# Kernel tuning notes

Hardware: AMD Instinct MI355X
Metric: run time of the kernel (lower is better)

## Reference

```python
import jax, jax.numpy as jnp
import numpy as np

B, T, C = 8, 2048, 512   # batch, seq_len, channels (= output_size for residual)
H, K, D = 4, 128, 128    # heads, key_size, per-head value size
KS, DIL = 4, 4           # conv kernel size, dilation = kernal_size**block_id
BAND = 3                 # matrix_band_part num_lower = num_upper = 3
NEG = -10000000.0


def setup_inputs() -> dict:
    key = jax.random.key(0)
    ks = jax.random.split(key, 12)
    s = 0.02
    f32 = jnp.float32
    x = jax.random.normal(ks[0], (B, T, C), f32)
    # per-head q/k/v dense params (stacked over head axis)
    Wq = jax.random.normal(ks[1], (H, C, K), f32) * s
    bq = jnp.zeros((H, K), f32)
    Wk = jax.random.normal(ks[2], (H, C, K), f32) * s
    bk = jnp.zeros((H, K), f32)
    Wv = jax.random.normal(ks[3], (H, C, D), f32) * s
    bv = jnp.zeros((H, D), f32)
    # output combiner Dense(output_size)
    Wo = jax.random.normal(ks[4], (H * D, C), f32) * s
    bo = jnp.zeros((C,), f32)
    # causal dilated Conv1D: kernel layout WIO = (kernel, in, out)
    Wc = jax.random.normal(ks[5], (KS, C, C), f32) * s
    bc = jnp.zeros((C,), f32)
    return {"x": x, "Wq": Wq, "bq": bq, "Wk": Wk, "bk": bk,
            "Wv": Wv, "bv": bv, "Wo": Wo, "bo": bo, "Wc": Wc, "bc": bc}


def reference(x, Wq, bq, Wk, bk, Wv, bv, Wo, bo, Wc, bc):
    # per-head projections: [B,H,T,K/D]
    q = jnp.einsum('btc,hck->bhtk', x, Wq) + bq[None, :, None, :]
    k = jnp.einsum('btc,hck->bhtk', x, Wk) + bk[None, :, None, :]
    v = jnp.einsum('btc,hcd->bhtd', x, Wv) + bv[None, :, None, :]
    # dense scores then band mask (faithful to matrix_band_part + abs>0 mask)
    sim = jnp.einsum('bhtk,bhsk->bhts', q, k) / jnp.sqrt(jnp.float32(K))
    idx = jnp.arange(T)
    band = (jnp.abs(idx[:, None] - idx[None, :]) <= BAND).astype(sim.dtype)
    simb = sim * band
    mask = jnp.where(jnp.abs(simb) > 0.0, 0.0, 1.0).astype(sim.dtype)
    att = jax.nn.softmax(simb + NEG * mask, axis=-1)
    heads = jnp.einsum('bhts,bhsd->bhtd', att, v)          # [B,H,T,D]
    cat = heads.transpose(0, 2, 1, 3).reshape(B, T, H * D)  # concat heads
    out = cat @ Wo + bo                                     # Dense(512)
    # causal dilated conv + relu
    pad = (KS - 1) * DIL
    conv = jax.lax.conv_general_dilated(
        out, Wc, window_strides=(1,), padding=[(pad, 0)],
        rhs_dilation=(DIL,), dimension_numbers=('NWC', 'WIO', 'NWC'))
    conv = jax.nn.relu(conv + bc)
    res = conv + x
    return jnp.where(res >= 0, res, 0.2 * res)  # leaky_relu(alpha=0.2)
```

## Files before the change

kernel.cpp:

```cpp
#include <hip/hip_runtime.h>
#include <math.h>

#define Bb    8
#define Tseq  2048
#define Cch   512
#define Mrows 16384
#define Nqkv  1536

typedef __bf16 bf16x8 __attribute__((ext_vector_type(8)));
typedef __bf16 bf16x4 __attribute__((ext_vector_type(4)));
typedef float  f32x4  __attribute__((ext_vector_type(4)));

__device__ __forceinline__ void gld_lds16(const void* g, void* l) {
  __builtin_amdgcn_global_load_lds(
      (const __attribute__((address_space(1))) unsigned int*)g,
      (__attribute__((address_space(3))) unsigned int*)l, 16, 0, 0);
}

#define SWZ(r, g) (((r) << 6) + ((((g) ^ ((r) & 7))) << 3))


__global__ __launch_bounds__(512, 2) void gemm_qkv_wp_kernel(
    const __bf16* __restrict__ xb, const __bf16* __restrict__ Wqkv_t,
    const float* __restrict__ bq, const float* __restrict__ bk,
    const float* __restrict__ bv, __bf16* __restrict__ qkv,
    const __bf16* __restrict__ Wc_t, const __bf16* __restrict__ Wob,
    __bf16* __restrict__ Wp_bt) {
  __shared__ __align__(16) __bf16 As[3][256 * 64];
  __shared__ __align__(16) __bf16 Bs[3][128 * 64];
  const int tid = threadIdx.x;
  const int w = tid >> 6, lane = tid & 63;
  const int wm = w & 3, wn = w >> 2;
  const int lm = lane & 15, quad = lane >> 4;
  const int srow = lane >> 3;
  const int scol = (((lane & 7) ^ srow) << 3);
  const int lid = blockIdx.x;

  const __bf16 *Ap, *Bp;
  __bf16* op;
  int lda, ldo, m0, n0;
  bool dobias;
  if (lid < 768) {
    const int xcd = lid & 7, chunk = lid >> 3;
    const int idx = xcd * 96 + chunk;
    const int mt = idx / 12, nt = idx - mt * 12;
    m0 = mt * 256; n0 = nt * 128;
    Ap = xb; lda = 512; Bp = Wqkv_t;
    op = qkv; ldo = 1536; dobias = true;
  } else {
    const int l2 = lid - 768;
    const int z = l2 >> 3, rest = l2 & 7;
    m0 = (rest >> 2) * 256; n0 = (rest & 3) * 128;
    Ap = Wc_t + z * 512; lda = 2048; Bp = Wob;
    op = Wp_bt + z * 512; ldo = 2048; dobias = false;
  }

  auto stage = [&](int buf, int t) {
    const int k0 = t * 64;
#pragma unroll
    for (int it = 0; it < 4; ++it) {
      const int c = w * 4 + it;
      gld_lds16(Ap + (size_t)(m0 + c * 8 + srow) * lda + k0 + scol,
                &As[buf][c * 512]);
    }
#pragma unroll
    for (int it = 0; it < 2; ++it) {
      const int c = w * 2 + it;
      gld_lds16(Bp + (size_t)(n0 + c * 8 + srow) * 512 + k0 + scol,
                &Bs[buf][c * 512]);
    }
  };

  f32x4 acc[4][4] = {};
  stage(0, 0);
  stage(1, 1);
  int bufc = 0;
  for (int t = 0; t < 8; ++t) {
    if (t < 7) asm volatile("s_waitcnt vmcnt(6)" ::: "memory");
    else       asm volatile("s_waitcnt vmcnt(0)" ::: "memory");
    __builtin_amdgcn_s_barrier();
    asm volatile("" ::: "memory");
    __builtin_amdgcn_s_setprio(1);
#pragma unroll
    for (int ks = 0; ks < 2; ++ks) {
      bf16x8 af[4], bfr[4];
#pragma unroll
      for (int i = 0; i < 4; ++i)
        af[i] = *(const bf16x8*)&As[bufc][SWZ(wm * 64 + i * 16 + lm, ks * 4 + quad)];
#pragma unroll
      for (int j = 0; j < 4; ++j)
        bfr[j] = *(const bf16x8*)&Bs[bufc][SWZ(wn * 64 + j * 16 + lm, ks * 4 + quad)];
#pragma unroll
      for (int i = 0; i < 4; ++i)
#pragma unroll
        for (int j = 0; j < 4; ++j)
          acc[i][j] = __builtin_amdgcn_mfma_f32_16x16x32_bf16(af[i], bfr[j], acc[i][j], 0, 0, 0);
    }
    __builtin_amdgcn_s_setprio(0);
    asm volatile("" ::: "memory");
    __builtin_amdgcn_s_barrier();
    asm volatile("" ::: "memory");
    if (t + 2 < 8) {
      int bn = bufc + 2; if (bn >= 3) bn -= 3;
      stage(bn, t + 2);
    }
    ++bufc; if (bufc == 3) bufc = 0;
  }
#pragma unroll
  for (int j = 0; j < 4; ++j) {
    const int col = n0 + wn * 64 + j * 16 + lm;
    float bias = 0.f;
    if (dobias) {
      const int s = col >> 9;
      const float* bp = (s == 0) ? bq : (s == 1 ? bk : bv);
      bias = bp[col & 511];
    }
#pragma unroll
    for (int i = 0; i < 4; ++i) {
      const int row0 = m0 + wm * 64 + i * 16 + quad * 4;
#pragma unroll
      for (int r = 0; r < 4; ++r)
        op[(size_t)(row0 + r) * ldo + col] = (__bf16)(acc[i][j][r] + bias);
    }
  }
}

__global__ __launch_bounds__(512, 2) void conv_gemm_kernel(
    const __bf16* __restrict__ A,
    const __bf16* __restrict__ Bt,
    const float* __restrict__ bc, const float* __restrict__ bj,
    const float* __restrict__ x, float* __restrict__ out,
    const __bf16* __restrict__ zeros) {
  __shared__ __align__(16) __bf16 As[3][256 * 64];
  __shared__ __align__(16) __bf16 Bs[3][128 * 64];
  const int tid = threadIdx.x;
  const int w = tid >> 6, lane = tid & 63;
  const int wm = w & 3, wn = w >> 2;
  const int lm = lane & 15, quad = lane >> 4;
  const int srow = lane >> 3;
  const int scol = (((lane & 7) ^ srow) << 3);
  const int lid = blockIdx.y * 4 + blockIdx.x;
  const int xcd = lid & 7, chunk = lid >> 3;
  const int idx = xcd * 32 + chunk;
  const int mt = idx >> 2, nt = idx & 3;
  const int m0 = mt * 256, n0 = nt * 128;

  auto stage = [&](int buf, int t) {
    const int k0 = t * 64;
    const int jtap = k0 >> 9;
    const int shift = 4 * jtap - 12;
    const int cin0 = k0 & 511;
#pragma unroll
    for (int it = 0; it < 4; ++it) {
      const int c = w * 4 + it;
      const int m = m0 + c * 8 + srow;
      const __bf16* src = (((m & (Tseq - 1)) + shift) >= 0)
                              ? A + (size_t)(m + shift) * Cch + cin0 + scol
                              : zeros + scol;
      gld_lds16(src, &As[buf][c * 512]);
    }
#pragma unroll
    for (int it = 0; it < 2; ++it) {
      const int c = w * 2 + it;
      gld_lds16(Bt + (size_t)(n0 + c * 8 + srow) * 2048 + k0 + scol,
                &Bs[buf][c * 512]);
    }
  };

  f32x4 acc[4][4] = {};
  stage(0, 0);
  stage(1, 1);
  int bufc = 0;
  for (int t = 0; t < 32; ++t) {
    if (t < 31) asm volatile("s_waitcnt vmcnt(6)" ::: "memory");
    else        asm volatile("s_waitcnt vmcnt(0)" ::: "memory");
    __builtin_amdgcn_s_barrier();
    asm volatile("" ::: "memory");
    __builtin_amdgcn_s_setprio(1);
#pragma unroll
    for (int ks = 0; ks < 2; ++ks) {
      bf16x8 af[4], bfr[4];
#pragma unroll
      for (int i = 0; i < 4; ++i)
        af[i] = *(const bf16x8*)&As[bufc][SWZ(wm * 64 + i * 16 + lm, ks * 4 + quad)];
#pragma unroll
      for (int j = 0; j < 4; ++j)
        bfr[j] = *(const bf16x8*)&Bs[bufc][SWZ(wn * 64 + j * 16 + lm, ks * 4 + quad)];
#pragma unroll
      for (int i = 0; i < 4; ++i)
#pragma unroll
        for (int j = 0; j < 4; ++j)
          acc[i][j] = __builtin_amdgcn_mfma_f32_16x16x32_bf16(af[i], bfr[j], acc[i][j], 0, 0, 0);
    }
    __builtin_amdgcn_s_setprio(0);
    asm volatile("" ::: "memory");
    __builtin_amdgcn_s_barrier();
    asm volatile("" ::: "memory");
    if (t + 2 < 32) {
      int bn = bufc + 2; if (bn >= 3) bn -= 3;
      stage(bn, t + 2);
    }
    ++bufc; if (bufc == 3) bufc = 0;
  }
#pragma unroll
  for (int j = 0; j < 4; ++j) {
    const int col = n0 + wn * 64 + j * 16 + lm;
    const float bcv = bc[col];
    float suf[4];
    suf[3] = bj[3 * 512 + col];
    suf[2] = suf[3] + bj[2 * 512 + col];
    suf[1] = suf[2] + bj[1 * 512 + col];
    suf[0] = suf[1] + bj[0 * 512 + col];
#pragma unroll
    for (int i = 0; i < 4; ++i) {
      const int row0 = m0 + wm * 64 + i * 16 + quad * 4;
#pragma unroll
      for (int r = 0; r < 4; ++r) {
        const int row = row0 + r;
        const int tl = row & (Tseq - 1);
        int jm = 15 - tl;
        jm = (jm < 0) ? 0 : (jm >> 2);
        float v = acc[i][j][r] + bcv + suf[jm];
        v = fmaxf(v, 0.f);
        v += x[(size_t)row * Cch + col];
        out[(size_t)row * Cch + col] = (v >= 0.f) ? v : 0.2f * v;
      }
    }
  }
}

__global__ __launch_bounds__(256) void attn_band_kernel(
    const __bf16* __restrict__ qkv, __bf16* __restrict__ cat) {
  __shared__ __align__(16) __bf16 ks[70 * 128];
  __shared__ __align__(16) __bf16 vs[70 * 128];
  const int tid = threadIdx.x;
  const int bh = blockIdx.y;
  const int b = bh >> 2, h = bh & 3;
  const int t0 = blockIdx.x * 64;
  for (int c = tid; c < 70 * 16; c += 256) {
    const int row = c >> 4, chunk = c & 15;
    int s = t0 - 3 + row;
    s = (s < 0) ? 0 : ((s > Tseq - 1) ? Tseq - 1 : s);
    const __bf16* src = qkv + ((size_t)(b * Tseq + s)) * Nqkv + 512 + h * 128 + chunk * 8;
    *(bf16x8*)&ks[row * 128 + chunk * 8] = *(const bf16x8*)src;
    *(bf16x8*)&vs[row * 128 + chunk * 8] = *(const bf16x8*)(src + 512);
  }
  __syncthreads();
  const int g = tid & 15, grp = tid >> 4;
  const int d0 = g * 8;
  const float scale = 0.08838834764831845f;
#pragma unroll
  for (int tt = 0; tt < 4; ++tt) {
    const int tl = grp * 4 + tt;
    const int t = t0 + tl;
    bf16x8 qv = *(const bf16x8*)(qkv + ((size_t)(b * Tseq + t)) * Nqkv + h * 128 + d0);
    float score[7];
#pragma unroll
    for (int i = 0; i < 7; ++i) {
      const int s = t - 3 + i;
      const bool valid = (s >= 0) && (s < Tseq);
      bf16x8 kv = *(const bf16x8*)&ks[(tl + i) * 128 + d0];
      float p = 0.f;
#pragma unroll
      for (int e = 0; e < 8; ++e) p += (float)qv[e] * (float)kv[e];
      p += __shfl_xor(p, 1);
      p += __shfl_xor(p, 2);
      p += __shfl_xor(p, 4);
      p += __shfl_xor(p, 8);
      score[i] = valid ? p * scale : -1e30f;
    }
    float mx = score[0];
#pragma unroll
    for (int i = 1; i < 7; ++i) mx = fmaxf(mx, score[i]);
    float wgt[7], denom = 0.f;
#pragma unroll
    for (int i = 0; i < 7; ++i) {
      wgt[i] = (score[i] > -1e29f) ? expf(score[i] - mx) : 0.f;
      denom += wgt[i];
    }
    const float inv = 1.f / denom;
    float o[8] = {};
#pragma unroll
    for (int i = 0; i < 7; ++i) {
      bf16x8 vv = *(const bf16x8*)&vs[(tl + i) * 128 + d0];
#pragma unroll
      for (int e = 0; e < 8; ++e) o[e] += wgt[i] * (float)vv[e];
    }
    bf16x8 ov;
#pragma unroll
    for (int e = 0; e < 8; ++e) ov[e] = (__bf16)(o[e] * inv);
    *(bf16x8*)(cat + ((size_t)(b * Tseq + t)) * Cch + h * 128 + d0) = ov;
  }
}

#define PREP_A 8192
#define PREP_B 8960
#define PREP_C 9984
#define PREP_D 10240
#define PREP_E 10241
#define PREP_N 10273

__global__ __launch_bounds__(256) void prep_kernel(
    const float* __restrict__ x, const float* __restrict__ Wq,
    const float* __restrict__ Wk, const float* __restrict__ Wv,
    const float* __restrict__ Wo, const float* __restrict__ Wc,
    const float* __restrict__ bo,
    __bf16* __restrict__ xb, __bf16* __restrict__ Wqkv_t,
    __bf16* __restrict__ Wc_t, __bf16* __restrict__ Wob,
    float* __restrict__ bj, __bf16* __restrict__ zeros) {
  __shared__ float sArr[32][33];
  __shared__ float red[256];
  const int bid = blockIdx.x;
  const int tid = threadIdx.x;
  if (bid < PREP_A) {
    const size_t i = ((size_t)bid * 256 + tid) * 4;
    float4 v = *(const float4*)(x + i);
    bf16x4 o;
    o[0] = (__bf16)v.x; o[1] = (__bf16)v.y; o[2] = (__bf16)v.z; o[3] = (__bf16)v.w;
    *(bf16x4*)(xb + i) = o;
  } else if (bid < PREP_B) {
    const int l = bid - PREP_A;
    const int bx = l & 3, by = (l >> 2) & 15, z = l >> 6;
    const int sgrp = z >> 2, h = z & 3;
    const float* src = ((sgrp == 0) ? Wq : (sgrp == 1) ? Wk : Wv) + h * (512 * 128);
    __bf16* dst = Wqkv_t + (size_t)z * 128 * 512;
    const int tx = tid & 31, ty = tid >> 5;
    const int c0 = bx * 32, r0 = by * 32;
#pragma unroll
    for (int rr = 0; rr < 4; ++rr)
      sArr[ty + rr * 8][tx] = src[(size_t)(r0 + ty + rr * 8) * 128 + c0 + tx];
    __syncthreads();
#pragma unroll
    for (int rr = 0; rr < 4; ++rr)
      dst[(size_t)(c0 + ty + rr * 8) * 512 + r0 + tx] = (__bf16)sArr[tx][ty + rr * 8];
  } else if (bid < PREP_C) {
    const int l = bid - PREP_B;
    const int bx = l & 15, by = l >> 4;
    const int tx = tid & 31, ty = tid >> 5;
    const int c0 = bx * 32, r0 = by * 32;
#pragma unroll
    for (int rr = 0; rr < 4; ++rr)
      sArr[ty + rr * 8][tx] = Wc[(size_t)(r0 + ty + rr * 8) * 512 + c0 + tx];
    __syncthreads();
#pragma unroll
    for (int rr = 0; rr < 4; ++rr)
      Wc_t[(size_t)(c0 + ty + rr * 8) * 2048 + r0 + tx] = (__bf16)sArr[tx][ty + rr * 8];
  } else if (bid < PREP_D) {
    const int l = bid - PREP_C;
    const size_t i = ((size_t)l * 256 + tid) * 4;
    float4 v = *(const float4*)(Wo + i);
    bf16x4 o;
    o[0] = (__bf16)v.x; o[1] = (__bf16)v.y; o[2] = (__bf16)v.z; o[3] = (__bf16)v.w;
    *(bf16x4*)(Wob + i) = o;
  } else if (bid < PREP_E) {
    bf16x8 zero = {};
    *(bf16x8*)(zeros + tid * 8) = zero;
  } else {
    const int l = bid - PREP_E;
    const int j = l >> 3, nb = l & 7;
    const int n = nb * 64 + (tid & 63);
    const int cig = tid >> 6;
    const float* base = Wc + ((size_t)j * 512 + cig * 128) * 512 + n;
    float acc = 0.f;
#pragma unroll 8
    for (int ci = 0; ci < 128; ++ci) acc += bo[cig * 128 + ci] * base[(size_t)ci * 512];
    red[tid] = acc;
    __syncthreads();
    if (tid < 64)
      bj[j * 512 + n] = red[tid] + red[tid + 64] + red[tid + 128] + red[tid + 192];
  }
}

extern "C" void kernel_launch(void* const* d_in, const int* in_sizes, int n_in,
                              void* d_out, int out_size, void* d_ws, size_t ws_size,
                              hipStream_t stream) {
  const float* x  = (const float*)d_in[0];
  const float* Wq = (const float*)d_in[1];
  const float* bq = (const float*)d_in[2];
  const float* Wk = (const float*)d_in[3];
  const float* bk = (const float*)d_in[4];
  const float* Wv = (const float*)d_in[5];
  const float* bv = (const float*)d_in[6];
  const float* Wo = (const float*)d_in[7];
  const float* bo = (const float*)d_in[8];
  const float* Wc = (const float*)d_in[9];
  const float* bc = (const float*)d_in[10];
  float* out = (float*)d_out;

  char* p = (char*)d_ws;
  __bf16* xb     = (__bf16*)p;  p += (size_t)Mrows * Cch * 2;
  __bf16* qkv    = (__bf16*)p;  p += (size_t)Mrows * Nqkv * 2;
  __bf16* catb   = (__bf16*)p;  p += (size_t)Mrows * Cch * 2;
  __bf16* Wqkv_t = (__bf16*)p;  p += (size_t)Nqkv * Cch * 2;
  __bf16* Wc_t   = (__bf16*)p;  p += (size_t)Cch * 2048 * 2;
  __bf16* Wob    = (__bf16*)p;  p += (size_t)Cch * Cch * 2;
  __bf16* Wp_bt  = (__bf16*)p;  p += (size_t)Cch * 2048 * 2;
  float*  bj     = (float*)p;   p += 4 * Cch * 4;
  __bf16* zeros  = (__bf16*)p;  p += 4096;

  prep_kernel<<<PREP_N, 256, 0, stream>>>(x, Wq, Wk, Wv, Wo, Wc, bo,
                                          xb, Wqkv_t, Wc_t, Wob, bj, zeros);

  gemm_qkv_wp_kernel<<<800, 512, 0, stream>>>(xb, Wqkv_t, bq, bk, bv, qkv,
                                              Wc_t, Wob, Wp_bt);

  attn_band_kernel<<<dim3(Tseq / 64, Bb * 4), 256, 0, stream>>>(qkv, catb);

  conv_gemm_kernel<<<dim3(Cch / 128, Mrows / 128 / 2), 512, 0, stream>>>(
      catb, Wp_bt, bc, bj, x, out, zeros);
}
```

Before: 224.7 us.

## Interleave LDS fragment loads, global prefetch and MFMA in sub-phases in GEMM kernels

```diff
diff --git a/kernel.cpp b/kernel.cpp
--- a/kernel.cpp
+++ b/kernel.cpp
@@ -18,9 +18,10 @@
 }
 
 #define SWZ(r, g) (((r) << 6) + ((((g) ^ ((r) & 7))) << 3))
-
-
-__global__ __launch_bounds__(512, 2) void gemm_qkv_wp_kernel(
+#define MFMA(d, a, b) d = __builtin_amdgcn_mfma_f32_16x16x32_bf16(a, b, d, 0, 0, 0)
+
+
+__global__ __launch_bounds__(512, 1) void gemm_qkv_wp_kernel(
     const __bf16* __restrict__ xb, const __bf16* __restrict__ Wqkv_t,
     const float* __restrict__ bq, const float* __restrict__ bk,
     const float* __restrict__ bv, __bf16* __restrict__ qkv,
@@ -55,14 +56,17 @@
     op = Wp_bt + z * 512; ldo = 2048; dobias = false;
   }
 
-  auto stage = [&](int buf, int t) {
+  auto stageA = [&](int buf, int t, int it0) {
     const int k0 = t * 64;
 #pragma unroll
-    for (int it = 0; it < 4; ++it) {
+    for (int it = it0; it < it0 + 2; ++it) {
       const int c = w * 4 + it;
       gld_lds16(Ap + (size_t)(m0 + c * 8 + srow) * lda + k0 + scol,
                 &As[buf][c * 512]);
     }
+  };
+  auto stageB = [&](int buf, int t) {
+    const int k0 = t * 64;
 #pragma unroll
     for (int it = 0; it < 2; ++it) {
       const int c = w * 2 + it;
@@ -72,39 +76,65 @@
   };
 
   f32x4 acc[4][4] = {};
-  stage(0, 0);
-  stage(1, 1);
-  int bufc = 0;
-  for (int t = 0; t < 8; ++t) {
-    if (t < 7) asm volatile("s_waitcnt vmcnt(6)" ::: "memory");
-    else       asm volatile("s_waitcnt vmcnt(0)" ::: "memory");
-    __builtin_amdgcn_s_barrier();
-    asm volatile("" ::: "memory");
+  stageA(0, 0, 0); stageA(0, 0, 2); stageB(0, 0);
+  stageA(1, 1, 0); stageA(1, 1, 2); stageB(1, 1);
+  asm volatile("s_waitcnt vmcnt(6)" ::: "memory");
+  __builtin_amdgcn_s_barrier();
+
+  const int NT = 8;
+  int st = 0;
+  for (int t = 0; t < NT; ++t) {
+    int sn = st + 2; if (sn >= 3) sn -= 3;
+    const bool pf = (t + 2 < NT);
+    bf16x8 a0[4], b0, b1;
+#pragma unroll
+    for (int i = 0; i < 4; ++i)
+      a0[i] = *(const bf16x8*)&As[st][SWZ(wm * 64 + i * 16 + lm, quad)];
+    b0 = *(const bf16x8*)&Bs[st][SWZ(wn * 64 + 0 * 16 + lm, quad)];
+    b1 = *(const bf16x8*)&Bs[st][SWZ(wn * 64 + 1 * 16 + lm, quad)];
+    if (pf) stageA(sn, t + 2, 0);
+    __builtin_amdgcn_s_barrier();
     __builtin_amdgcn_s_setprio(1);
 #pragma unroll
-    for (int ks = 0; ks < 2; ++ks) {
-      bf16x8 af[4], bfr[4];
-#pragma unroll
-      for (int i = 0; i < 4; ++i)
-        af[i] = *(const bf16x8*)&As[bufc][SWZ(wm * 64 + i * 16 + lm, ks * 4 + quad)];
-#pragma unroll
-      for (int j = 0; j < 4; ++j)
-        bfr[j] = *(const bf16x8*)&Bs[bufc][SWZ(wn * 64 + j * 16 + lm, ks * 4 + quad)];
-#pragma unroll
-      for (int i = 0; i < 4; ++i)
-#pragma unroll
-        for (int j = 0; j < 4; ++j)
-          acc[i][j] = __builtin_amdgcn_mfma_f32_16x16x32_bf16(af[i], bfr[j], acc[i][j], 0, 0, 0);
-    }
+    for (int i = 0; i < 4; ++i) { MFMA(acc[i][0], a0[i], b0); MFMA(acc[i][1], a0[i], b1); }
     __builtin_amdgcn_s_setprio(0);
-    asm volatile("" ::: "memory");
-    __builtin_amdgcn_s_barrier();
-    asm volatile("" ::: "memory");
-    if (t + 2 < 8) {
-      int bn = bufc + 2; if (bn >= 3) bn -= 3;
-      stage(bn, t + 2);
-    }
-    ++bufc; if (bufc == 3) bufc = 0;
+    __builtin_amdgcn_s_barrier();
+    {
+      bf16x8 b2 = *(const bf16x8*)&Bs[st][SWZ(wn * 64 + 2 * 16 + lm, quad)];
+      bf16x8 b3 = *(const bf16x8*)&Bs[st][SWZ(wn * 64 + 3 * 16 + lm, quad)];
+      if (pf) stageA(sn, t + 2, 2);
+      __builtin_amdgcn_s_barrier();
+      __builtin_amdgcn_s_setprio(1);
+#pragma unroll
+      for (int i = 0; i < 4; ++i) { MFMA(acc[i][2], a0[i], b2); MFMA(acc[i][3], a0[i], b3); }
+      __builtin_amdgcn_s_setprio(0);
+      __builtin_amdgcn_s_barrier();
+    }
+    bf16x8 a1[4], c0, c1;
+#pragma unroll
+    for (int i = 0; i < 4; ++i)
+      a1[i] = *(const bf16x8*)&As[st][SWZ(wm * 64 + i * 16 + lm, 4 + quad)];
+    c0 = *(const bf16x8*)&Bs[st][SWZ(wn * 64 + 0 * 16 + lm, 4 + quad)];
+    c1 = *(const bf16x8*)&Bs[st][SWZ(wn * 64 + 1 * 16 + lm, 4 + quad)];
+    if (pf) stageB(sn, t + 2);
+    __builtin_amdgcn_s_barrier();
+    __builtin_amdgcn_s_setprio(1);
+#pragma unroll
+    for (int i = 0; i < 4; ++i) { MFMA(acc[i][0], a1[i], c0); MFMA(acc[i][1], a1[i], c1); }
+    __builtin_amdgcn_s_setprio(0);
+    __builtin_amdgcn_s_barrier();
+    {
+      bf16x8 c2 = *(const bf16x8*)&Bs[st][SWZ(wn * 64 + 2 * 16 + lm, 4 + quad)];
+      bf16x8 c3 = *(const bf16x8*)&Bs[st][SWZ(wn * 64 + 3 * 16 + lm, 4 + quad)];
+      __builtin_amdgcn_s_setprio(1);
+#pragma unroll
+      for (int i = 0; i < 4; ++i) { MFMA(acc[i][2], a1[i], c2); MFMA(acc[i][3], a1[i], c3); }
+      __builtin_amdgcn_s_setprio(0);
+    }
+    if (t < NT - 2)       asm volatile("s_waitcnt vmcnt(6)" ::: "memory");
+    else if (t == NT - 2) asm volatile("s_waitcnt vmcnt(0)" ::: "memory");
+    if (t < NT - 1) __builtin_amdgcn_s_barrier();
+    ++st; if (st == 3) st = 0;
   }
 #pragma unroll
   for (int j = 0; j < 4; ++j) {
@@ -125,7 +155,7 @@
   }
 }
 
-__global__ __launch_bounds__(512, 2) void conv_gemm_kernel(
+__global__ __launch_bounds__(512, 1) void conv_gemm_kernel(
     const __bf16* __restrict__ A,
     const __bf16* __restrict__ Bt,
     const float* __restrict__ bc, const float* __restrict__ bj,
@@ -145,13 +175,13 @@
   const int mt = idx >> 2, nt = idx & 3;
   const int m0 = mt * 256, n0 = nt * 128;
 
-  auto stage = [&](int buf, int t) {
+  auto stageA = [&](int buf, int t, int it0) {
     const int k0 = t * 64;
     const int jtap = k0 >> 9;
     const int shift = 4 * jtap - 12;
     const int cin0 = k0 & 511;
 #pragma unroll
-    for (int it = 0; it < 4; ++it) {
+    for (int it = it0; it < it0 + 2; ++it) {
       const int c = w * 4 + it;
       const int m = m0 + c * 8 + srow;
       const __bf16* src = (((m & (Tseq - 1)) + shift) >= 0)
@@ -159,6 +189,9 @@
                               : zeros + scol;
       gld_lds16(src, &As[buf][c * 512]);
     }
+  };
+  auto stageB = [&](int buf, int t) {
+    const int k0 = t * 64;
 #pragma unroll
     for (int it = 0; it < 2; ++it) {
       const int c = w * 2 + it;
@@ -168,39 +201,65 @@
   };
 
   f32x4 acc[4][4] = {};
-  stage(0, 0);
-  stage(1, 1);
-  int bufc = 0;
-  for (int t = 0; t < 32; ++t) {
-    if (t < 31) asm volatile("s_waitcnt vmcnt(6)" ::: "memory");
-    else        asm volatile("s_waitcnt vmcnt(0)" ::: "memory");
-    __builtin_amdgcn_s_barrier();
-    asm volatile("" ::: "memory");
+  stageA(0, 0, 0); stageA(0, 0, 2); stageB(0, 0);
+  stageA(1, 1, 0); stageA(1, 1, 2); stageB(1, 1);
+  asm volatile("s_waitcnt vmcnt(6)" ::: "memory");
+  __builtin_amdgcn_s_barrier();
+
+  const int NT = 32;
+  int st = 0;
+  for (int t = 0; t < NT; ++t) {
+    int sn = st + 2; if (sn >= 3) sn -= 3;
+    const bool pf = (t + 2 < NT);
+    bf16x8 a0[4], b0, b1;
+#pragma unroll
+    for (int i = 0; i < 4; ++i)
+      a0[i] = *(const bf16x8*)&As[st][SWZ(wm * 64 + i * 16 + lm, quad)];
+    b0 = *(const bf16x8*)&Bs[st][SWZ(wn * 64 + 0 * 16 + lm, quad)];
+    b1 = *(const bf16x8*)&Bs[st][SWZ(wn * 64 + 1 * 16 + lm, quad)];
+    if (pf) stageA(sn, t + 2, 0);
+    __builtin_amdgcn_s_barrier();
     __builtin_amdgcn_s_setprio(1);
 #pragma unroll
-    for (int ks = 0; ks < 2; ++ks) {
-      bf16x8 af[4], bfr[4];
-#pragma unroll
-      for (int i = 0; i < 4; ++i)
-        af[i] = *(const bf16x8*)&As[bufc][SWZ(wm * 64 + i * 16 + lm, ks * 4 + quad)];
-#pragma unroll
-      for (int j = 0; j < 4; ++j)
-        bfr[j] = *(const bf16x8*)&Bs[bufc][SWZ(wn * 64 + j * 16 + lm, ks * 4 + quad)];
-#pragma unroll
-      for (int i = 0; i < 4; ++i)
-#pragma unroll
-        for (int j = 0; j < 4; ++j)
-          acc[i][j] = __builtin_amdgcn_mfma_f32_16x16x32_bf16(af[i], bfr[j], acc[i][j], 0, 0, 0);
-    }
+    for (int i = 0; i < 4; ++i) { MFMA(acc[i][0], a0[i], b0); MFMA(acc[i][1], a0[i], b1); }
     __builtin_amdgcn_s_setprio(0);
-    asm volatile("" ::: "memory");
-    __builtin_amdgcn_s_barrier();
-    asm volatile("" ::: "memory");
-    if (t + 2 < 32) {
-      int bn = bufc + 2; if (bn >= 3) bn -= 3;
-      stage(bn, t + 2);
-    }
-    ++bufc; if (bufc == 3) bufc = 0;
+    __builtin_amdgcn_s_barrier();
+    {
+      bf16x8 b2 = *(const bf16x8*)&Bs[st][SWZ(wn * 64 + 2 * 16 + lm, quad)];
+      bf16x8 b3 = *(const bf16x8*)&Bs[st][SWZ(wn * 64 + 3 * 16 + lm, quad)];
+      if (pf) stageA(sn, t + 2, 2);
+      __builtin_amdgcn_s_barrier();
+      __builtin_amdgcn_s_setprio(1);
+#pragma unroll
+      for (int i = 0; i < 4; ++i) { MFMA(acc[i][2], a0[i], b2); MFMA(acc[i][3], a0[i], b3); }
+      __builtin_amdgcn_s_setprio(0);
+      __builtin_amdgcn_s_barrier();
+    }
+    bf16x8 a1[4], c0, c1;
+#pragma unroll
+    for (int i = 0; i < 4; ++i)
+      a1[i] = *(const bf16x8*)&As[st][SWZ(wm * 64 + i * 16 + lm, 4 + quad)];
+    c0 = *(const bf16x8*)&Bs[st][SWZ(wn * 64 + 0 * 16 + lm, 4 + quad)];
+    c1 = *(const bf16x8*)&Bs[st][SWZ(wn * 64 + 1 * 16 + lm, 4 + quad)];
+    if (pf) stageB(sn, t + 2);
+    __builtin_amdgcn_s_barrier();
+    __builtin_amdgcn_s_setprio(1);
+#pragma unroll
+    for (int i = 0; i < 4; ++i) { MFMA(acc[i][0], a1[i], c0); MFMA(acc[i][1], a1[i], c1); }
+    __builtin_amdgcn_s_setprio(0);
+    __builtin_amdgcn_s_barrier();
+    {
+      bf16x8 c2 = *(const bf16x8*)&Bs[st][SWZ(wn * 64 + 2 * 16 + lm, 4 + quad)];
+      bf16x8 c3 = *(const bf16x8*)&Bs[st][SWZ(wn * 64 + 3 * 16 + lm, 4 + quad)];
+      __builtin_amdgcn_s_setprio(1);
+#pragma unroll
+      for (int i = 0; i < 4; ++i) { MFMA(acc[i][2], a1[i], c2); MFMA(acc[i][3], a1[i], c3); }
+      __builtin_amdgcn_s_setprio(0);
+    }
+    if (t < NT - 2)       asm volatile("s_waitcnt vmcnt(6)" ::: "memory");
+    else if (t == NT - 2) asm volatile("s_waitcnt vmcnt(0)" ::: "memory");
+    if (t < NT - 1) __builtin_amdgcn_s_barrier();
+    ++st; if (st == 3) st = 0;
   }
 #pragma unroll
   for (int j = 0; j < 4; ++j) {
```

After: 226.4 us. About the same (+0.8%).
